# Kernel tuning notes

Measured on AMD Instinct MI355X. Metric: run time of the kernel, lower is better.

The kernel has to match this reference:

```python
import jax, jax.numpy as jnp
import numpy as np

GROUPS = 52
B, C, H, W = 16, 52, 256, 256  # c must equal groups (see t_value.view(b, c, 1, 1) in source)


def setup_inputs() -> dict:
    key = jax.random.key(0)
    ks = jax.random.split(key, 4)
    x = jax.random.normal(ks[0], (B, C, H, W), jnp.float32)
    weight = jax.random.normal(ks[1], (1, GROUPS, 1, 1), jnp.float32) * 0.1
    bias = jnp.ones((1, GROUPS, 1, 1), jnp.float32)
    one = jnp.ones((1, GROUPS, 1), jnp.float32)
    zero = jax.random.normal(ks[2], (1, GROUPS, 1), jnp.float32) * 0.1
    theta = jax.random.uniform(ks[3], (1, 2, 1, 1), jnp.float32)
    scale = jnp.ones((1,), jnp.float32)
    return dict(x=x, weight=weight, bias=bias, one=one, zero=zero, theta=theta, scale=scale)


def _prm_forward(x, weight, bias, one, zero, theta, scale):
    b, c, h, w = x.shape
    G = GROUPS
    cpg = c // G  # == 1 (required by original code)
    bg, hw = b * G, h * w

    xv = x.reshape(bg, cpg, hw)                      # [bg, cpg, hw]
    value = xv.sum(axis=1)                           # per-group channel-sum map [bg, hw]

    # adaptive max pool with indices (row-major argmax, first occurrence, same as torch)
    idx = jnp.argmax(value, axis=1)                  # [bg]
    qrow = (idx // w).astype(x.dtype)                # [bg]
    qcol = (idx % w).astype(x.dtype)                 # [bg]
    qval = jnp.take_along_axis(value, idx[:, None], axis=1)  # [bg, 1] == query_value

    # tiny per-group similarity matmuls (contraction over cpg)
    sim_max = jnp.einsum('gc,gch->gh', qval, xv)     # [bg, hw]
    gap = x.mean(axis=(2, 3)).reshape(bg, cpg)       # global avg pool per group-channel
    sim_gap = jnp.einsum('gc,gch->gh', gap, xv)      # [bg, hw]

    # positional Gaussian weighting: Normal(0, scale).log_prob(d * theta).exp()
    sigma = scale[0]
    log_norm = -jnp.log(sigma) - 0.5 * jnp.log(2.0 * jnp.pi)

    def gpdf(z):
        return jnp.exp(-0.5 * (z / sigma) ** 2 + log_norm)

    rows = jnp.arange(h, dtype=x.dtype)
    cols = jnp.arange(w, dtype=x.dtype)
    dr = jnp.abs(rows[None, :, None] - qrow[:, None, None])   # [bg, h, 1]
    dc = jnp.abs(cols[None, None, :] - qcol[:, None, None])   # [bg, 1, w]
    # mean over the 2 coordinate channels; broadcast avoids materializing [bg,2,h,w]
    dist = 0.5 * (gpdf(dr * theta[0, 0, 0, 0]) + gpdf(dc * theta[0, 1, 0, 0]))  # [bg, h, w]

    sim_max = sim_max.reshape(b, G, hw) * dist.reshape(b, G, hw)
    sim_gap = sim_gap.reshape(b, G, hw)
    sim = sim_max * zero + sim_gap * one             # [b, G, hw]

    # spatial mean/std normalization (torch .std -> ddof=1)
    ctx = sim - sim.mean(axis=2, keepdims=True)
    std = jnp.std(ctx, axis=2, keepdims=True, ddof=1) + 1e-05
    ctx = (ctx / std).reshape(b, G, h, w) * weight + bias

    # broadcast per-group gate over the group's channels, then sigmoid gate
    ctx = jnp.broadcast_to(ctx.reshape(bg, 1, h, w), (bg, cpg, h, w)).reshape(b, c, h, w)
    return x * jax.nn.sigmoid(ctx)


def reference(x, weight, bias, one, zero, theta, scale):
    return _prm_forward(x, weight, bias, one, zero, theta, scale)
```

## Files before the change

kernel.cpp:

```cpp
#include <hip/hip_runtime.h>
#include <math.h>

#define Gn 52
#define Hn 256
#define Wn 256
#define HW (Hn * Wn)
#define HW4 (HW / 4)
#define BG 832
#define TPB 1024
#define VPT 16

typedef float vf4 __attribute__((ext_vector_type(4)));

__global__ __launch_bounds__(TPB, 4) void k_fused(
    const float4* __restrict__ x4,
    const float* __restrict__ weight, const float* __restrict__ bias,
    const float* __restrict__ one_,  const float* __restrict__ zero,
    const float* __restrict__ theta, const float* __restrict__ scale,
    float4* __restrict__ out4)
{
    const int bg   = blockIdx.x;
    const int g    = bg % Gn;
    const int t    = threadIdx.x;
    const int wave = t >> 6;
    const int lane = t & 63;
    const size_t base4 = (size_t)bg * HW4;
    const float4* xp = x4 + base4;

    __shared__ float rv[16];
    __shared__ int   ri[16];
    __shared__ float r1[16];
    __shared__ float r2[16];
    __shared__ float bc[6];
    __shared__ float wcol[256];
    __shared__ float urow[256];

    float4 v[VPT];
    #pragma unroll
    for (int k = 0; k < VPT; ++k) v[k] = xp[t + k * TPB];

    float vmaxA = -INFINITY, vmaxB = -INFINITY;
    int   imaxA = 0x7fffffff, imaxB = 0x7fffffff;
    float sumA = 0.f, sumB = 0.f;
    #pragma unroll
    for (int k = 0; k < VPT; k += 2) {
        int e0 = (t + k * TPB) * 4;
        float4 q0 = v[k];
        sumA += (q0.x + q0.y) + (q0.z + q0.w);
        if (q0.x > vmaxA) { vmaxA = q0.x; imaxA = e0; }
        if (q0.y > vmaxA) { vmaxA = q0.y; imaxA = e0 + 1; }
        if (q0.z > vmaxA) { vmaxA = q0.z; imaxA = e0 + 2; }
        if (q0.w > vmaxA) { vmaxA = q0.w; imaxA = e0 + 3; }
        int e1 = (t + (k + 1) * TPB) * 4;
        float4 q1 = v[k + 1];
        sumB += (q1.x + q1.y) + (q1.z + q1.w);
        if (q1.x > vmaxB) { vmaxB = q1.x; imaxB = e1; }
        if (q1.y > vmaxB) { vmaxB = q1.y; imaxB = e1 + 1; }
        if (q1.z > vmaxB) { vmaxB = q1.z; imaxB = e1 + 2; }
        if (q1.w > vmaxB) { vmaxB = q1.w; imaxB = e1 + 3; }
    }
    float sum = sumA + sumB;
    float vmax = vmaxA; int imax = imaxA;
    if (vmaxB > vmax || (vmaxB == vmax && imaxB < imax)) { vmax = vmaxB; imax = imaxB; }
    #pragma unroll
    for (int off = 32; off > 0; off >>= 1) {
        float ov = __shfl_down(vmax, off);
        int   oi = __shfl_down(imax, off);
        float os = __shfl_down(sum,  off);
        sum += os;
        if (ov > vmax || (ov == vmax && oi < imax)) { vmax = ov; imax = oi; }
    }
    if (lane == 0) { rv[wave] = vmax; ri[wave] = imax; r1[wave] = sum; }
    __syncthreads();
    if (t < 64) {
        float bv = (t < 16) ? rv[t] : -INFINITY;
        int   bi = (t < 16) ? ri[t] : 0x7fffffff;
        float bs = (t < 16) ? r1[t] : 0.f;
        #pragma unroll
        for (int off = 8; off > 0; off >>= 1) {
            float ov = __shfl_down(bv, off);
            int   oi = __shfl_down(bi, off);
            float os = __shfl_down(bs, off);
            bs += os;
            if (ov > bv || (ov == bv && oi < bi)) { bv = ov; bi = oi; }
        }
        if (t == 0) {
            bc[0] = bv;
            bc[1] = (float)(bi >> 8);
            bc[2] = (float)(bi & 255);
            bc[3] = bs * (1.f / (float)HW);
        }
    }
    __syncthreads();

    const float sigma   = scale[0];
    const float inv2s2  = 0.5f / (sigma * sigma);
    const float lognorm = -logf(sigma) - 0.9189385332046727f;
    const float A   = zero[g] * bc[0];
    const float Bc  = one_[g] * bc[3];
    const float A05 = 0.5f * A;
    if (t < 256) {
        float zc = ((float)t - bc[2]) * theta[1];
        wcol[t] = A05 * __expf(lognorm - zc * zc * inv2s2);
    } else if (t < 512) {
        float zr = ((float)(t - 256) - bc[1]) * theta[0];
        urow[t - 256] = A05 * __expf(lognorm - zr * zr * inv2s2) + Bc;
    }
    __syncthreads();

    const float4 cw = *reinterpret_cast<const float4*>(&wcol[(t & 63) << 2]);

    float s1 = 0.f, s2 = 0.f;
    #pragma unroll
    for (int k = 0; k < VPT; ++k) {
        const float ur = urow[wave + 16 * k];
        float4 q = v[k];
        float f, sim;
        f = ur + cw.x; sim = f * q.x; s1 += sim; s2 = fmaf(sim, sim, s2);
        f = ur + cw.y; sim = f * q.y; s1 += sim; s2 = fmaf(sim, sim, s2);
        f = ur + cw.z; sim = f * q.z; s1 += sim; s2 = fmaf(sim, sim, s2);
        f = ur + cw.w; sim = f * q.w; s1 += sim; s2 = fmaf(sim, sim, s2);
    }
    #pragma unroll
    for (int off = 32; off > 0; off >>= 1) {
        s1 += __shfl_down(s1, off);
        s2 += __shfl_down(s2, off);
    }
    if (lane == 0) { r1[wave] = s1; r2[wave] = s2; }
    __syncthreads();
    if (t < 64) {
        float S1 = (t < 16) ? r1[t] : 0.f;
        float S2 = (t < 16) ? r2[t] : 0.f;
        #pragma unroll
        for (int off = 8; off > 0; off >>= 1) {
            S1 += __shfl_down(S1, off);
            S2 += __shfl_down(S2, off);
        }
        if (t == 0) {
            float mean = S1 * (1.f / (float)HW);
            float var  = (S2 - S1 * mean) * (1.f / (float)(HW - 1));
            var = fmaxf(var, 0.f);
            bc[4] = mean;
            bc[5] = weight[g] / (sqrtf(var) + 1e-5f);
        }
    }
    __syncthreads();
    const float mean = bc[4], wsc = bc[5];
    const float wb = fmaf(-mean, wsc, bias[g]);

    #pragma unroll
    for (int k = 0; k < VPT; ++k) {
        const float ur = urow[wave + 16 * k];
        float4 q = v[k];
        vf4 o;
        {
            float f = ur + cw.x, sim = f * q.x;
            float ctx = fmaf(sim, wsc, wb);
            o.x = q.x * __builtin_amdgcn_rcpf(1.f + __expf(-ctx));
        }
        {
            float f = ur + cw.y, sim = f * q.y;
            float ctx = fmaf(sim, wsc, wb);
            o.y = q.y * __builtin_amdgcn_rcpf(1.f + __expf(-ctx));
        }
        {
            float f = ur + cw.z, sim = f * q.z;
            float ctx = fmaf(sim, wsc, wb);
            o.z = q.z * __builtin_amdgcn_rcpf(1.f + __expf(-ctx));
        }
        {
            float f = ur + cw.w, sim = f * q.w;
            float ctx = fmaf(sim, wsc, wb);
            o.w = q.w * __builtin_amdgcn_rcpf(1.f + __expf(-ctx));
        }
        __builtin_nontemporal_store(o, reinterpret_cast<vf4*>(out4 + base4 + t + k * TPB));
    }
}

extern "C" void kernel_launch(void* const* d_in, const int* in_sizes, int n_in,
                              void* d_out, int out_size, void* d_ws, size_t ws_size,
                              hipStream_t stream) {
    const float* x      = (const float*)d_in[0];
    const float* weight = (const float*)d_in[1];
    const float* bias   = (const float*)d_in[2];
    const float* one_   = (const float*)d_in[3];
    const float* zero   = (const float*)d_in[4];
    const float* theta  = (const float*)d_in[5];
    const float* scale  = (const float*)d_in[6];
    float* out = (float*)d_out;

    k_fused<<<BG, TPB, 0, stream>>>((const float4*)x, weight, bias, one_, zero,
                                    theta, scale, (float4*)out);
}
```

Baseline: 390.0 us.

## Process four slices per persistent block and prefetch next slice into LDS

Each block now handles four consecutive (batch,group) slices instead of one, and the grid shrinks from one block per slice to a quarter of that. While a slice is being processed, part of the next slice is prefetched into LDS with async global_load_lds, and the rest is loaded directly into registers, overlapping memory traffic with the reductions and barriers. This targets the latency exposed by the serial reduce-barrier chain in each slice, but a block now uses about 144KB of LDS, which may cap occupancy at one block per CU, and the hand-written waitcnt ordering is fragile.

```diff
diff --git a/kernel.cpp b/kernel.cpp
--- a/kernel.cpp
+++ b/kernel.cpp
@@ -6,11 +6,20 @@
 #define Wn 256
 #define HW (Hn * Wn)
 #define HW4 (HW / 4)
-#define BG 832
+#define NSLICE 832
+#define NBLK 208
+#define NPER 4
 #define TPB 1024
 #define VPT 16
+#define LCH 9
 
 typedef float vf4 __attribute__((ext_vector_type(4)));
+typedef __attribute__((address_space(3))) unsigned int lds_u32;
+typedef __attribute__((address_space(1))) const unsigned int glb_u32;
+
+#define BAR() do { asm volatile("s_waitcnt lgkmcnt(0)" ::: "memory"); \
+                   __builtin_amdgcn_s_barrier();                      \
+                   asm volatile("" ::: "memory"); } while (0)
 
 __global__ __launch_bounds__(TPB, 4) void k_fused(
     const float4* __restrict__ x4,
@@ -19,161 +28,176 @@
     const float* __restrict__ theta, const float* __restrict__ scale,
     float4* __restrict__ out4)
 {
-    const int bg   = blockIdx.x;
-    const int g    = bg % Gn;
-    const int t    = threadIdx.x;
-    const int wave = t >> 6;
-    const int lane = t & 63;
-    const size_t base4 = (size_t)bg * HW4;
-    const float4* xp = x4 + base4;
-
+    __shared__ float4 lds4[LCH * TPB];
+    __shared__ __align__(16) float wcol[256];
+    __shared__ float urow[256];
     __shared__ float rv[16];
     __shared__ int   ri[16];
     __shared__ float r1[16];
     __shared__ float r2[16];
-    __shared__ float bc[6];
-    __shared__ float wcol[256];
-    __shared__ float urow[256];
-
-    float4 v[VPT];
-    #pragma unroll
-    for (int k = 0; k < VPT; ++k) v[k] = xp[t + k * TPB];
-
-    float vmaxA = -INFINITY, vmaxB = -INFINITY;
-    int   imaxA = 0x7fffffff, imaxB = 0x7fffffff;
-    float sumA = 0.f, sumB = 0.f;
-    #pragma unroll
-    for (int k = 0; k < VPT; k += 2) {
-        int e0 = (t + k * TPB) * 4;
-        float4 q0 = v[k];
-        sumA += (q0.x + q0.y) + (q0.z + q0.w);
-        if (q0.x > vmaxA) { vmaxA = q0.x; imaxA = e0; }
-        if (q0.y > vmaxA) { vmaxA = q0.y; imaxA = e0 + 1; }
-        if (q0.z > vmaxA) { vmaxA = q0.z; imaxA = e0 + 2; }
-        if (q0.w > vmaxA) { vmaxA = q0.w; imaxA = e0 + 3; }
-        int e1 = (t + (k + 1) * TPB) * 4;
-        float4 q1 = v[k + 1];
-        sumB += (q1.x + q1.y) + (q1.z + q1.w);
-        if (q1.x > vmaxB) { vmaxB = q1.x; imaxB = e1; }
-        if (q1.y > vmaxB) { vmaxB = q1.y; imaxB = e1 + 1; }
-        if (q1.z > vmaxB) { vmaxB = q1.z; imaxB = e1 + 2; }
-        if (q1.w > vmaxB) { vmaxB = q1.w; imaxB = e1 + 3; }
-    }
-    float sum = sumA + sumB;
-    float vmax = vmaxA; int imax = imaxA;
-    if (vmaxB > vmax || (vmaxB == vmax && imaxB < imax)) { vmax = vmaxB; imax = imaxB; }
-    #pragma unroll
-    for (int off = 32; off > 0; off >>= 1) {
-        float ov = __shfl_down(vmax, off);
-        int   oi = __shfl_down(imax, off);
-        float os = __shfl_down(sum,  off);
-        sum += os;
-        if (ov > vmax || (ov == vmax && oi < imax)) { vmax = ov; imax = oi; }
-    }
-    if (lane == 0) { rv[wave] = vmax; ri[wave] = imax; r1[wave] = sum; }
-    __syncthreads();
-    if (t < 64) {
-        float bv = (t < 16) ? rv[t] : -INFINITY;
-        int   bi = (t < 16) ? ri[t] : 0x7fffffff;
-        float bs = (t < 16) ? r1[t] : 0.f;
-        #pragma unroll
-        for (int off = 8; off > 0; off >>= 1) {
-            float ov = __shfl_down(bv, off);
-            int   oi = __shfl_down(bi, off);
-            float os = __shfl_down(bs, off);
-            bs += os;
-            if (ov > bv || (ov == bv && oi < bi)) { bv = ov; bi = oi; }
-        }
-        if (t == 0) {
-            bc[0] = bv;
-            bc[1] = (float)(bi >> 8);
-            bc[2] = (float)(bi & 255);
-            bc[3] = bs * (1.f / (float)HW);
-        }
-    }
-    __syncthreads();
+    __shared__ float bc[2];
+
+    const int t    = threadIdx.x;
+    const int wave = t >> 6;
+    const int lane = t & 63;
 
     const float sigma   = scale[0];
     const float inv2s2  = 0.5f / (sigma * sigma);
     const float lognorm = -logf(sigma) - 0.9189385332046727f;
-    const float A   = zero[g] * bc[0];
-    const float Bc  = one_[g] * bc[3];
-    const float A05 = 0.5f * A;
-    if (t < 256) {
-        float zc = ((float)t - bc[2]) * theta[1];
-        wcol[t] = A05 * __expf(lognorm - zc * zc * inv2s2);
-    } else if (t < 512) {
-        float zr = ((float)(t - 256) - bc[1]) * theta[0];
-        urow[t - 256] = A05 * __expf(lognorm - zr * zr * inv2s2) + Bc;
-    }
-    __syncthreads();
-
-    const float4 cw = *reinterpret_cast<const float4*>(&wcol[(t & 63) << 2]);
-
-    float s1 = 0.f, s2 = 0.f;
+    const float th0 = theta[0], th1 = theta[1];
+
     #pragma unroll
-    for (int k = 0; k < VPT; ++k) {
-        const float ur = urow[wave + 16 * k];
-        float4 q = v[k];
-        float f, sim;
-        f = ur + cw.x; sim = f * q.x; s1 += sim; s2 = fmaf(sim, sim, s2);
-        f = ur + cw.y; sim = f * q.y; s1 += sim; s2 = fmaf(sim, sim, s2);
-        f = ur + cw.z; sim = f * q.z; s1 += sim; s2 = fmaf(sim, sim, s2);
-        f = ur + cw.w; sim = f * q.w; s1 += sim; s2 = fmaf(sim, sim, s2);
-    }
-    #pragma unroll
-    for (int off = 32; off > 0; off >>= 1) {
-        s1 += __shfl_down(s1, off);
-        s2 += __shfl_down(s2, off);
-    }
-    if (lane == 0) { r1[wave] = s1; r2[wave] = s2; }
-    __syncthreads();
-    if (t < 64) {
-        float S1 = (t < 16) ? r1[t] : 0.f;
-        float S2 = (t < 16) ? r2[t] : 0.f;
-        #pragma unroll
-        for (int off = 8; off > 0; off >>= 1) {
-            S1 += __shfl_down(S1, off);
-            S2 += __shfl_down(S2, off);
-        }
-        if (t == 0) {
-            float mean = S1 * (1.f / (float)HW);
-            float var  = (S2 - S1 * mean) * (1.f / (float)(HW - 1));
-            var = fmaxf(var, 0.f);
-            bc[4] = mean;
-            bc[5] = weight[g] / (sqrtf(var) + 1e-5f);
-        }
-    }
-    __syncthreads();
-    const float mean = bc[4], wsc = bc[5];
-    const float wb = fmaf(-mean, wsc, bias[g]);
-
-    #pragma unroll
-    for (int k = 0; k < VPT; ++k) {
-        const float ur = urow[wave + 16 * k];
-        float4 q = v[k];
-        vf4 o;
-        {
-            float f = ur + cw.x, sim = f * q.x;
-            float ctx = fmaf(sim, wsc, wb);
+    for (int it = 0; it < NPER; ++it) {
+        const int bg = blockIdx.x * NPER + it;
+        const int g  = bg % Gn;
+        const size_t base4 = (size_t)bg * HW4;
+        const float4* xp = x4 + base4;
+
+        float4 v[VPT];
+        if (it == 0) {
+            #pragma unroll
+            for (int k = 0; k < VPT; ++k) v[k] = xp[t + k * TPB];
+        } else {
+            asm volatile("s_waitcnt vmcnt(16)" ::: "memory");
+            __builtin_amdgcn_sched_barrier(0);
+            #pragma unroll
+            for (int k = 0; k < LCH; ++k) v[k] = lds4[k * TPB + t];
+            #pragma unroll
+            for (int k = LCH; k < VPT; ++k) v[k] = xp[t + k * TPB];
+            asm volatile("s_waitcnt lgkmcnt(0)" ::: "memory");
+            __builtin_amdgcn_sched_barrier(0);
+        }
+        if (it + 1 < NPER) {
+            const float4* xn = x4 + (size_t)(bg + 1) * HW4;
+            #pragma unroll
+            for (int k = 0; k < LCH; ++k) {
+                __builtin_amdgcn_global_load_lds(
+                    (glb_u32*)(xn + k * TPB + t),
+                    (lds_u32*)&lds4[k * TPB + (t & ~63)], 16, 0, 0);
+            }
+        }
+
+        float vmaxA = -INFINITY, vmaxB = -INFINITY;
+        int   imaxA = 0x7fffffff, imaxB = 0x7fffffff;
+        float sumA = 0.f, sumB = 0.f;
+        #pragma unroll
+        for (int k = 0; k < VPT; k += 2) {
+            int e0 = (t + k * TPB) * 4;
+            float4 q0 = v[k];
+            sumA += (q0.x + q0.y) + (q0.z + q0.w);
+            if (q0.x > vmaxA) { vmaxA = q0.x; imaxA = e0; }
+            if (q0.y > vmaxA) { vmaxA = q0.y; imaxA = e0 + 1; }
+            if (q0.z > vmaxA) { vmaxA = q0.z; imaxA = e0 + 2; }
+            if (q0.w > vmaxA) { vmaxA = q0.w; imaxA = e0 + 3; }
+            int e1 = (t + (k + 1) * TPB) * 4;
+            float4 q1 = v[k + 1];
+            sumB += (q1.x + q1.y) + (q1.z + q1.w);
+            if (q1.x > vmaxB) { vmaxB = q1.x; imaxB = e1; }
+            if (q1.y > vmaxB) { vmaxB = q1.y; imaxB = e1 + 1; }
+            if (q1.z > vmaxB) { vmaxB = q1.z; imaxB = e1 + 2; }
+            if (q1.w > vmaxB) { vmaxB = q1.w; imaxB = e1 + 3; }
+        }
+        float sum = sumA + sumB;
+        float vmax = vmaxA; int imax = imaxA;
+        if (vmaxB > vmax || (vmaxB == vmax && imaxB < imax)) { vmax = vmaxB; imax = imaxB; }
+        #pragma unroll
+        for (int off = 32; off > 0; off >>= 1) {
+            float ov = __shfl_down(vmax, off);
+            int   oi = __shfl_down(imax, off);
+            float os = __shfl_down(sum,  off);
+            sum += os;
+            if (ov > vmax || (ov == vmax && oi < imax)) { vmax = ov; imax = oi; }
+        }
+        if (lane == 0) { rv[wave] = vmax; ri[wave] = imax; r1[wave] = sum; }
+        BAR();
+
+        if (wave == 0) {
+            float bv = (lane < 16) ? rv[lane] : -INFINITY;
+            int   bi = (lane < 16) ? ri[lane] : 0x7fffffff;
+            float bs = (lane < 16) ? r1[lane] : 0.f;
+            #pragma unroll
+            for (int off = 8; off > 0; off >>= 1) {
+                float ov = __shfl_down(bv, off);
+                int   oi = __shfl_down(bi, off);
+                float os = __shfl_down(bs, off);
+                bs += os;
+                if (ov > bv || (ov == bv && oi < bi)) { bv = ov; bi = oi; }
+            }
+            bv = __shfl(bv, 0); bi = __shfl(bi, 0); bs = __shfl(bs, 0);
+            const float qrow = (float)(bi >> 8);
+            const float qcol = (float)(bi & 255);
+            const float A05  = 0.5f * zero[g] * bv;
+            const float Bc   = one_[g] * (bs * (1.f / (float)HW));
+            #pragma unroll
+            for (int j = 0; j < 4; ++j) {
+                int c = (lane << 2) + j;
+                float zc = ((float)c - qcol) * th1;
+                wcol[c] = A05 * __expf(lognorm - zc * zc * inv2s2);
+                float zr = ((float)c - qrow) * th0;
+                urow[c] = A05 * __expf(lognorm - zr * zr * inv2s2) + Bc;
+            }
+        }
+        BAR();
+
+        const float4 cw = *reinterpret_cast<const float4*>(&wcol[lane << 2]);
+
+        float s1 = 0.f, s2 = 0.f;
+        #pragma unroll
+        for (int k = 0; k < VPT; ++k) {
+            const float ur = urow[16 * k + wave];
+            float4 q = v[k];
+            float f, sim;
+            f = ur + cw.x; sim = f * q.x; s1 += sim; s2 = fmaf(sim, sim, s2);
+            f = ur + cw.y; sim = f * q.y; s1 += sim; s2 = fmaf(sim, sim, s2);
+            f = ur + cw.z; sim = f * q.z; s1 += sim; s2 = fmaf(sim, sim, s2);
+            f = ur + cw.w; sim = f * q.w; s1 += sim; s2 = fmaf(sim, sim, s2);
+        }
+        #pragma unroll
+        for (int off = 32; off > 0; off >>= 1) {
+            s1 += __shfl_down(s1, off);
+            s2 += __shfl_down(s2, off);
+        }
+        if (lane == 0) { r1[wave] = s1; r2[wave] = s2; }
+        BAR();
+
+        if (wave == 0) {
+            float S1 = (lane < 16) ? r1[lane] : 0.f;
+            float S2 = (lane < 16) ? r2[lane] : 0.f;
+            #pragma unroll
+            for (int off = 8; off > 0; off >>= 1) {
+                S1 += __shfl_down(S1, off);
+                S2 += __shfl_down(S2, off);
+            }
+            if (lane == 0) {
+                float mean = S1 * (1.f / (float)HW);
+                float var  = (S2 - S1 * mean) * (1.f / (float)(HW - 1));
+                var = fmaxf(var, 0.f);
+                bc[0] = mean;
+                bc[1] = weight[g] / (sqrtf(var) + 1e-5f);
+            }
+        }
+        BAR();
+
+        const float mean = bc[0], wsc = bc[1];
+        const float wb = fmaf(-mean, wsc, bias[g]);
+
+        #pragma unroll
+        for (int k = 0; k < VPT; ++k) {
+            const float ur = urow[16 * k + wave];
+            float4 q = v[k];
+            vf4 o;
+            float f, sim, ctx;
+            f = ur + cw.x; sim = f * q.x; ctx = fmaf(sim, wsc, wb);
             o.x = q.x * __builtin_amdgcn_rcpf(1.f + __expf(-ctx));
-        }
-        {
-            float f = ur + cw.y, sim = f * q.y;
-            float ctx = fmaf(sim, wsc, wb);
+            f = ur + cw.y; sim = f * q.y; ctx = fmaf(sim, wsc, wb);
             o.y = q.y * __builtin_amdgcn_rcpf(1.f + __expf(-ctx));
-        }
-        {
-            float f = ur + cw.z, sim = f * q.z;
-            float ctx = fmaf(sim, wsc, wb);
+            f = ur + cw.z; sim = f * q.z; ctx = fmaf(sim, wsc, wb);
             o.z = q.z * __builtin_amdgcn_rcpf(1.f + __expf(-ctx));
-        }
-        {
-            float f = ur + cw.w, sim = f * q.w;
-            float ctx = fmaf(sim, wsc, wb);
+            f = ur + cw.w; sim = f * q.w; ctx = fmaf(sim, wsc, wb);
             o.w = q.w * __builtin_amdgcn_rcpf(1.f + __expf(-ctx));
-        }
-        __builtin_nontemporal_store(o, reinterpret_cast<vf4*>(out4 + base4 + t + k * TPB));
+            __builtin_nontemporal_store(o,
+                reinterpret_cast<vf4*>(out4 + base4 + t + k * TPB));
+        }
     }
 }
 
@@ -189,6 +213,6 @@
     const float* scale  = (const float*)d_in[6];
     float* out = (float*)d_out;
 
-    k_fused<<<BG, TPB, 0, stream>>>((const float4*)x, weight, bias, one_, zero,
-                                    theta, scale, (float4*)out);
+    k_fused<<<NBLK, TPB, 0, stream>>>((const float4*)x, weight, bias, one_, zero,
+                                      theta, scale, (float4*)out);
 }
```

After: 387.9 us. About the same (-0.5%).
